# Optimization experiments

Measured on AMD Instinct MI355X. Metric: run time of the kernel, lower is better.

Reference implementation:

```python
import jax, jax.numpy as jnp
import numpy as np
from jax import lax

B, T, H, W, C = 2, 16, 64, 64, 64
KT, K = 3, 3


def kernel_to_freq_3d(kernel, T, H, W):
    # kernel: (C, k_t, k_h, k_w) -> (C, T, H, W) complex freq response
    Cc, k_t, k_h, k_w = kernel.shape
    t_idx = (jnp.arange(k_t) - k_t // 2) % T
    h_idx = (jnp.arange(k_h) - k_h // 2) % H
    w_idx = (jnp.arange(k_w) - k_w // 2) % W
    tt, th, tw = jnp.meshgrid(t_idx, h_idx, w_idx, indexing='ij')
    padded = jnp.zeros((Cc, T, H, W), dtype=kernel.dtype).at[:, tt, th, tw].set(kernel)
    return jnp.fft.fftn(padded, axes=(1, 2, 3))


def mamba_op(left, right):
    a1, b1 = left
    a2, b2 = right
    return (a1 * a2, a2 * b1 + b2)


def setup_inputs() -> dict:
    key = jax.random.key(0)
    ks = jax.random.split(key, 8)
    fan_in = KT * K * K
    x = jax.random.normal(ks[0], (B, T, H, W, C), dtype=jnp.float32)
    A_kernel = jax.random.normal(ks[1], (C, KT, K, K), dtype=jnp.float32) / np.sqrt(fan_in)
    B_kernel = jax.random.normal(ks[2], (C, KT, K, K), dtype=jnp.float32) / np.sqrt(fan_in)
    forget_bias = jnp.full((C,), 2.0, dtype=jnp.float32)
    forget_scale = jnp.full((C,), 0.01, dtype=jnp.float32)
    input_bias = jnp.zeros((C,), dtype=jnp.float32)
    input_scale = jnp.full((C,), 0.01, dtype=jnp.float32)
    delta_W = jax.random.normal(ks[3], (C, C), dtype=jnp.float32) / np.sqrt(C)
    delta_b = jnp.zeros((C,), dtype=jnp.float32)
    return {"x": x, "A_kernel": A_kernel, "B_kernel": B_kernel,
            "forget_bias": forget_bias, "forget_scale": forget_scale,
            "input_bias": input_bias, "input_scale": input_scale,
            "delta_W": delta_W, "delta_b": delta_b}


def reference(x, A_kernel, B_kernel, forget_bias, forget_scale,
              input_bias, input_scale, delta_W, delta_b):
    Bb, Tt, Hh, Ww, Cc = x.shape
    # freq-domain kernels: (C,T,H,W) -> (T,1,H,W,C) for broadcasting over batch
    A_f = kernel_to_freq_3d(A_kernel, Tt, Hh, Ww).transpose(1, 2, 3, 0)[:, None]
    B_f = kernel_to_freq_3d(B_kernel, Tt, Hh, Ww).transpose(1, 2, 3, 0)[:, None]
    # input-dependent gates (real, elementwise per channel)
    forget_gate = jax.nn.sigmoid(forget_bias + forget_scale * x)
    input_gate = jax.nn.sigmoid(input_bias + input_scale * x)
    delta = jax.nn.softplus(jnp.einsum('bthwc,cd->bthwd', x, delta_W) + delta_b)
    x_f = jnp.fft.fftn(x, axes=(1, 2, 3))  # complex (B,T,H,W,C)
    # move time axis to front for the scan: (T,B,H,W,C)
    a_seq = forget_gate.transpose(1, 0, 2, 3, 4) * A_f
    b_seq = (input_gate.transpose(1, 0, 2, 3, 4)
             * delta.transpose(1, 0, 2, 3, 4)
             * B_f * x_f.transpose(1, 0, 2, 3, 4))
    _, h_all_f = lax.associative_scan(mamba_op, (a_seq, b_seq), axis=0)
    h_f = h_all_f.transpose(1, 0, 2, 3, 4)
    h = jnp.fft.ifftn(h_f, axes=(1, 2, 3)).real
    return h.astype(x.dtype)
```

## Files before the change

### kernel.cpp

```cpp
#include <hip/hip_runtime.h>
#include <math.h>

#define Bb 2
#define Tt 16
#define Hh 64
#define Ww 64
#define Cc 64
#define ST_ (Hh*Ww*Cc)
#define SH_ (Ww*Cc)
#define SB_ (Tt*Hh*Ww*Cc)
#define XELEMS (Bb*Tt*Hh*Ww*Cc)

#define TWO_PI 6.2831853071795864769f

typedef __attribute__((ext_vector_type(8))) short bf16x8;
typedef __attribute__((ext_vector_type(4))) float f32x4;

#define OFF_PRE  8388608u
#define OFF_TWF  8390656u
#define OFF_THF  8394752u
#define OFF_THI  8402944u
#define OFF_TWI  8411136u

__device__ __forceinline__ float2 cmul(float2 a, float2 b) {
    return make_float2(fmaf(a.x, b.x, -a.y * b.y), fmaf(a.x, b.y, a.y * b.x));
}
__device__ __forceinline__ float2 cadd(float2 a, float2 b) { return make_float2(a.x + b.x, a.y + b.y); }
__device__ __forceinline__ float2 csub(float2 a, float2 b) { return make_float2(a.x - b.x, a.y - b.y); }

__device__ __forceinline__ unsigned bfpack(float2 f) {
    unsigned r = __float_as_uint(f.x);
    unsigned i = __float_as_uint(f.y);
    r = (r + 0x7fffu + ((r >> 16) & 1u)) >> 16;
    i = (i + 0x7fffu + ((i >> 16) & 1u)) >> 16;
    return r | (i << 16);
}
__device__ __forceinline__ float2 bfunpack(unsigned u) {
    return make_float2(__uint_as_float(u << 16), __uint_as_float(u & 0xffff0000u));
}

template <int S>
__device__ __forceinline__ void fft4(float2& a, float2& b, float2& c, float2& d) {
    float2 t0 = cadd(a, c), t1 = csub(a, c);
    float2 t2 = cadd(b, d), t3 = csub(b, d);
    a = cadd(t0, t2);
    c = csub(t0, t2);
    b = make_float2(t1.x - (float)S * t3.y, t1.y + (float)S * t3.x);
    d = make_float2(t1.x + (float)S * t3.y, t1.y - (float)S * t3.x);
}

template <int S>
__device__ __forceinline__ void fft16(float2 v[16]) {
    const float CS[10] = {1.f, 0.92387953f, 0.70710678f, 0.38268343f, 0.f,
                          -0.38268343f, -0.70710678f, -0.92387953f, -1.f, -0.92387953f};
    const float SN[10] = {0.f, 0.38268343f, 0.70710678f, 0.92387953f, 1.f,
                          0.92387953f, 0.70710678f, 0.38268343f, 0.f, -0.38268343f};
    float2 A[4][4];
#pragma unroll
    for (int j = 0; j < 4; ++j) {
        A[j][0] = v[j]; A[j][1] = v[4 + j]; A[j][2] = v[8 + j]; A[j][3] = v[12 + j];
        fft4<S>(A[j][0], A[j][1], A[j][2], A[j][3]);
#pragma unroll
        for (int k0 = 0; k0 < 4; ++k0) {
            int m = j * k0;
            float2 tw = make_float2(CS[m], (float)S * SN[m]);
            A[j][k0] = cmul(A[j][k0], tw);
        }
    }
#pragma unroll
    for (int k0 = 0; k0 < 4; ++k0) {
        fft4<S>(A[0][k0], A[1][k0], A[2][k0], A[3][k0]);
        v[k0] = A[0][k0]; v[k0 + 4] = A[1][k0]; v[k0 + 8] = A[2][k0]; v[k0 + 12] = A[3][k0];
    }
}

__global__ __launch_bounds__(256) void k_setup(const float* __restrict__ dW,
                                               unsigned* __restrict__ ws) {
    int j = blockIdx.x * 256 + threadIdx.x;
    if (j < 2048) {
        int p2 = j & 3, lane = (j >> 2) & 63, ka = (j >> 8) & 1, nt = j >> 9;
        int kb = ka * 32 + (lane >> 4) * 8 + 2 * p2;
        int ccol = (lane & 15) + 16 * nt;
        ws[OFF_PRE + j] = bfpack(make_float2(dW[kb * 64 + ccol], dW[(kb + 1) * 64 + ccol]));
        return;
    }
    int idx, table;
    if (j < 6144)       { idx = j - 2048;  table = 0; }
    else if (j < 14336) { idx = j - 6144;  table = 1; }
    else if (j < 22528) { idx = j - 14336; table = 2; }
    else                { idx = j - 22528; table = 3; }
    int p = idx & 3;
    int lane = (idx >> 2) & 63;
    int m = lane & 15, q = lane >> 4;
    int ka, r, reim;
    if (table == 0)      { ka = (idx >> 8) & 1; r = (idx >> 9) & 3;  reim = (idx >> 11) & 1; }
    else if (table == 3) { ka = (idx >> 8) & 3; r = (idx >> 10) & 3; reim = 0; }
    else                 { ka = (idx >> 8) & 3; r = (idx >> 10) & 3; reim = (idx >> 12) & 1; }
    int wp = r * 16 + m;
    int k0 = ka * 32 + q * 8 + 2 * p;
    float val[2];
#pragma unroll
    for (int dk = 0; dk < 2; ++dk) {
        int k = k0 + dk;
        float v;
        if (table == 0) {
            int a = (wp * k) & 63;
            float sn, cs; sincosf(TWO_PI * (float)a * (1.0f / 64.0f), &sn, &cs);
            v = (reim == 0) ? cs : -sn;
        } else {
            int h = k >> 1;
            int a = (wp * h) & 63;
            float sn, cs; sincosf(TWO_PI * (float)a * (1.0f / 64.0f), &sn, &cs);
            bool even = (k & 1) == 0;
            if (table == 1) {
                v = (reim == 0) ? (even ? cs : sn) : (even ? -sn : cs);
            } else if (table == 2) {
                v = (reim == 0) ? (even ? cs : -sn) : (even ? sn : cs);
                v *= (1.0f / 64.0f);
            } else {
                v = (even ? cs : -sn) * (1.0f / 64.0f);
            }
        }
        val[dk] = v;
    }
    unsigned base = (table == 0) ? OFF_TWF : (table == 1) ? OFF_THF
                  : (table == 2) ? OFF_THI : OFF_TWI;
    ws[base + idx] = bfpack(make_float2(val[0], val[1]));
}

__global__ __launch_bounds__(256) void k_dft_w_fwd(const float* __restrict__ x,
                                                   unsigned* __restrict__ X,
                                                   const uint4* __restrict__ T) {
    __shared__ float xsl[64 * 65];
    int tid = threadIdx.x;
    int sbase = blockIdx.x * 4096;
    for (int i = tid; i < 4096; i += 256)
        xsl[(i >> 6) * 65 + (i & 63)] = x[sbase + i];
    __syncthreads();

    int r = tid >> 6, lane = tid & 63;
    int m = lane & 15, q = lane >> 4;
    union U48 { uint4 u4; unsigned u[4]; bf16x8 v8; };
    U48 Are[2], Aim[2], Bf;
#pragma unroll
    for (int ka = 0; ka < 2; ++ka) {
        Are[ka].u4 = T[((0 * 4 + r) * 2 + ka) * 64 + lane];
        Aim[ka].u4 = T[((1 * 4 + r) * 2 + ka) * 64 + lane];
    }
    f32x4 ar[4], ai[4];
#pragma unroll
    for (int nt = 0; nt < 4; ++nt) { ar[nt] = (f32x4){0.f,0.f,0.f,0.f}; ai[nt] = (f32x4){0.f,0.f,0.f,0.f}; }
#pragma unroll
    for (int nt = 0; nt < 4; ++nt) {
        int cc = m + 16 * nt;
#pragma unroll
        for (int ka = 0; ka < 2; ++ka) {
            int w0 = ka * 32 + q * 8;
#pragma unroll
            for (int p = 0; p < 4; ++p)
                Bf.u[p] = bfpack(make_float2(xsl[(w0 + 2 * p) * 65 + cc],
                                             xsl[(w0 + 2 * p + 1) * 65 + cc]));
            ar[nt] = __builtin_amdgcn_mfma_f32_16x16x32_bf16(Are[ka].v8, Bf.v8, ar[nt], 0, 0, 0);
            ai[nt] = __builtin_amdgcn_mfma_f32_16x16x32_bf16(Aim[ka].v8, Bf.v8, ai[nt], 0, 0, 0);
        }
    }
#pragma unroll
    for (int nt = 0; nt < 4; ++nt) {
        int cc = m + 16 * nt;
#pragma unroll
        for (int reg = 0; reg < 4; ++reg) {
            int wp = r * 16 + q * 4 + reg;
            X[sbase + wp * 64 + cc] = bfpack(make_float2(ar[nt][reg], ai[nt][reg]));
        }
    }
}

__global__ __launch_bounds__(256) void k_dft_h(unsigned* __restrict__ X,
                                               const uint4* __restrict__ T) {
    __shared__ unsigned zs[64 * 68];
    int tid = threadIdx.x;
    int s = blockIdx.x;
    int bt = s >> 6, w = s & 63;
    int base = bt * ST_ + w * 64;
    for (int i = tid; i < 4096; i += 256)
        zs[(i >> 6) * 68 + (i & 63)] = X[base + (i >> 6) * SH_ + (i & 63)];
    __syncthreads();

    int r = tid >> 6, lane = tid & 63;
    int m = lane & 15, q = lane >> 4;
    union U48 { uint4 u4; unsigned u[4]; bf16x8 v8; };
    U48 Are[4], Aim[4], Bf;
#pragma unroll
    for (int ka = 0; ka < 4; ++ka) {
        Are[ka].u4 = T[((0 * 4 + r) * 4 + ka) * 64 + lane];
        Aim[ka].u4 = T[((1 * 4 + r) * 4 + ka) * 64 + lane];
    }
    f32x4 ar[4], ai[4];
#pragma unroll
    for (int nt = 0; nt < 4; ++nt) { ar[nt] = (f32x4){0.f,0.f,0.f,0.f}; ai[nt] = (f32x4){0.f,0.f,0.f,0.f}; }
#pragma unroll
    for (int nt = 0; nt < 4; ++nt) {
        int cc = m + 16 * nt;
#pragma unroll
        for (int ka = 0; ka < 4; ++ka) {
            int h0 = ka * 16 + q * 4;
            Bf.u[0] = zs[(h0 + 0) * 68 + cc];
            Bf.u[1] = zs[(h0 + 1) * 68 + cc];
            Bf.u[2] = zs[(h0 + 2) * 68 + cc];
            Bf.u[3] = zs[(h0 + 3) * 68 + cc];
            ar[nt] = __builtin_amdgcn_mfma_f32_16x16x32_bf16(Are[ka].v8, Bf.v8, ar[nt], 0, 0, 0);
            ai[nt] = __builtin_amdgcn_mfma_f32_16x16x32_bf16(Aim[ka].v8, Bf.v8, ai[nt], 0, 0, 0);
        }
    }
#pragma unroll
    for (int nt = 0; nt < 4; ++nt) {
        int cc = m + 16 * nt;
#pragma unroll
        for (int reg = 0; reg < 4; ++reg) {
            int hp = r * 16 + q * 4 + reg;
            X[base + hp * SH_ + cc] = bfpack(make_float2(ar[nt][reg], ai[nt][reg]));
        }
    }
}

__global__ __launch_bounds__(256) void k_dft_w_inv(const unsigned* __restrict__ X,
                                                   float* __restrict__ out,
                                                   const uint4* __restrict__ T) {
    __shared__ unsigned zs[64 * 68];
    int tid = threadIdx.x;
    int sbase = blockIdx.x * 4096;
    for (int i = tid; i < 4096; i += 256)
        zs[(i >> 6) * 68 + (i & 63)] = X[sbase + i];
    __syncthreads();

    int r = tid >> 6, lane = tid & 63;
    int m = lane & 15, q = lane >> 4;
    union U48 { uint4 u4; unsigned u[4]; bf16x8 v8; };
    U48 Are[4], Bf;
#pragma unroll
    for (int ka = 0; ka < 4; ++ka)
        Are[ka].u4 = T[(r * 4 + ka) * 64 + lane];
    f32x4 ar[4];
#pragma unroll
    for (int nt = 0; nt < 4; ++nt) ar[nt] = (f32x4){0.f,0.f,0.f,0.f};
#pragma unroll
    for (int nt = 0; nt < 4; ++nt) {
        int cc = m + 16 * nt;
#pragma unroll
        for (int ka = 0; ka < 4; ++ka) {
            int w0 = ka * 16 + q * 4;
            Bf.u[0] = zs[(w0 + 0) * 68 + cc];
            Bf.u[1] = zs[(w0 + 1) * 68 + cc];
            Bf.u[2] = zs[(w0 + 2) * 68 + cc];
            Bf.u[3] = zs[(w0 + 3) * 68 + cc];
            ar[nt] = __builtin_amdgcn_mfma_f32_16x16x32_bf16(Are[ka].v8, Bf.v8, ar[nt], 0, 0, 0);
        }
    }
#pragma unroll
    for (int nt = 0; nt < 4; ++nt) {
        int cc = m + 16 * nt;
#pragma unroll
        for (int reg = 0; reg < 4; ++reg) {
            int wp = r * 16 + q * 4 + reg;
            out[sbase + wp * 64 + cc] = ar[nt][reg];
        }
    }
}

__global__ __launch_bounds__(256) void k_mid(
    const float* __restrict__ x, unsigned* __restrict__ X,
    const float* __restrict__ Ak, const float* __restrict__ Bk,
    const float* __restrict__ fb, const float* __restrict__ fs,
    const float* __restrict__ ib, const float* __restrict__ isc_,
    const uint4* __restrict__ pre, const float* __restrict__ db) {
    const float CT[16] = {1.f, 0.9238795f, 0.7071068f, 0.3826834f, 0.f, -0.3826834f,
                          -0.7071068f, -0.9238795f, -1.f, -0.9238795f, -0.7071068f,
                          -0.3826834f, 0.f, 0.3826834f, 0.7071068f, 0.9238795f};
    const float SN[16] = {0.f, 0.3826834f, 0.7071068f, 0.9238795f, 1.f, 0.9238795f,
                          0.7071068f, 0.3826834f, 0.f, -0.3826834f, -0.7071068f,
                          -0.9238795f, -1.f, -0.9238795f, -0.7071068f, -0.3826834f};
    __shared__ float Akl[1728], Bkl[1728];
    __shared__ __align__(16) float xs[4][16 * 68 + 4];

    int tid = threadIdx.x;
    int g = tid >> 6, lane = tid & 63;
    int c = lane;
    int site = blockIdx.x * 4 + g;
    int b = site >> 12, hw = site & 4095;
    int h = hw >> 6, w = hw & 63;
    int base = b * SB_ + hw * 64;

    for (int i = tid; i < 1728; i += 256) { Akl[i] = Ak[i]; Bkl[i] = Bk[i]; }

    float xv[16];
    float2 v[16];
#pragma unroll
    for (int t = 0; t < 16; ++t) {
        xv[t] = x[base + t * ST_ + c];
        v[t] = bfunpack(X[base + t * ST_ + c]);
    }
#pragma unroll
    for (int t = 0; t < 16; ++t) xs[g][t * 68 + c] = xv[t];
    __syncthreads();

    int m = lane & 15, q = lane >> 4;
    bf16x8 Afrag[2];
#pragma unroll
    for (int ka = 0; ka < 2; ++ka) {
        int d0 = ka * 32 + q * 8;
        const float* p = &xs[g][m * 68 + d0];
        float4 f0 = *(const float4*)p;
        float4 f1 = *(const float4*)(p + 4);
        union { bf16x8 v8; unsigned u[4]; } U;
        U.u[0] = bfpack(make_float2(f0.x, f0.y));
        U.u[1] = bfpack(make_float2(f0.z, f0.w));
        U.u[2] = bfpack(make_float2(f1.x, f1.y));
        U.u[3] = bfpack(make_float2(f1.z, f1.w));
        Afrag[ka] = U.v8;
    }
#pragma unroll
    for (int nt = 0; nt < 4; ++nt) {
        int ccol = m + 16 * nt;
        float dbn = db[ccol];
        f32x4 acc = {dbn, dbn, dbn, dbn};
#pragma unroll
        for (int ka = 0; ka < 2; ++ka) {
            union { bf16x8 v8; uint4 u4; } Ub;
            Ub.u4 = pre[(nt * 2 + ka) * 64 + lane];
            acc = __builtin_amdgcn_mfma_f32_16x16x32_bf16(Afrag[ka], Ub.v8, acc, 0, 0, 0);
        }
#pragma unroll
        for (int reg = 0; reg < 4; ++reg)
            xs[g][(q * 4 + reg) * 68 + ccol] = acc[reg];
    }

    float sh, ch; sincosf(TWO_PI * (float)h / 64.0f, &sh, &ch);
    float sw, cw; sincosf(TWO_PI * (float)w / 64.0f, &sw, &cw);
    float2 eh[3] = { make_float2(ch, sh), make_float2(1.f, 0.f), make_float2(ch, -sh) };
    float2 ew[3] = { make_float2(cw, sw), make_float2(1.f, 0.f), make_float2(cw, -sw) };
    float2 GA[3], GB[3];
#pragma unroll
    for (int kt = 0; kt < 3; ++kt) { GA[kt] = make_float2(0.f, 0.f); GB[kt] = make_float2(0.f, 0.f); }
#pragma unroll
    for (int kh = 0; kh < 3; ++kh) {
#pragma unroll
        for (int kw = 0; kw < 3; ++kw) {
            float2 e = cmul(eh[kh], ew[kw]);
#pragma unroll
            for (int kt = 0; kt < 3; ++kt) {
                float ka = Akl[c * 27 + kt * 9 + kh * 3 + kw];
                float kb = Bkl[c * 27 + kt * 9 + kh * 3 + kw];
                GA[kt].x = fmaf(ka, e.x, GA[kt].x);
                GA[kt].y = fmaf(ka, e.y, GA[kt].y);
                GB[kt].x = fmaf(kb, e.x, GB[kt].x);
                GB[kt].y = fmaf(kb, e.y, GB[kt].y);
            }
        }
    }
    float fbc = fb[c], fsc = fs[c], ibc = ib[c], iscv = isc_[c];

    fft16<-1>(v);
    __syncthreads();

    float delta_raw[16];
#pragma unroll
    for (int t = 0; t < 16; ++t) delta_raw[t] = xs[g][t * 68 + c];

    float2 hv = make_float2(0.f, 0.f);
#pragma unroll
    for (int t = 0; t < 16; ++t) {
        float ct = CT[t], st = SN[t];
        float2 Af, Bf;
        Af.x = GA[1].x + ct * (GA[0].x + GA[2].x) - st * (GA[0].y - GA[2].y);
        Af.y = GA[1].y + ct * (GA[0].y + GA[2].y) + st * (GA[0].x - GA[2].x);
        Bf.x = GB[1].x + ct * (GB[0].x + GB[2].x) - st * (GB[0].y - GB[2].y);
        Bf.y = GB[1].y + ct * (GB[0].y + GB[2].y) + st * (GB[0].x - GB[2].x);

        float xc = xv[t];
        float fg  = __builtin_amdgcn_rcpf(1.f + __expf(-(fbc + fsc * xc)));
        float igv = __builtin_amdgcn_rcpf(1.f + __expf(-(ibc + iscv * xc)));
        float dot = delta_raw[t];
        float delta = (dot > 20.f) ? dot : __logf(1.f + __expf(dot));

        float sR = igv * delta;
        float2 bbv;
        bbv.x = sR * (Bf.x * v[t].x - Bf.y * v[t].y);
        bbv.y = sR * (Bf.x * v[t].y + Bf.y * v[t].x);
        float2 av = make_float2(fg * Af.x, fg * Af.y);
        float2 nh;
        nh.x = av.x * hv.x - av.y * hv.y + bbv.x;
        nh.y = av.x * hv.y + av.y * hv.x + bbv.y;
        hv = nh;
        v[t] = hv;
    }

    fft16<1>(v);

#pragma unroll
    for (int t = 0; t < 16; ++t) {
        float2 o = make_float2(v[t].x * 0.0625f, v[t].y * 0.0625f);
        X[base + t * ST_ + c] = bfpack(o);
    }
}

extern "C" void kernel_launch(void* const* d_in, const int* in_sizes, int n_in,
                              void* d_out, int out_size, void* d_ws, size_t ws_size,
                              hipStream_t stream) {
    const float* x   = (const float*)d_in[0];
    const float* Ak  = (const float*)d_in[1];
    const float* Bk  = (const float*)d_in[2];
    const float* fb  = (const float*)d_in[3];
    const float* fs  = (const float*)d_in[4];
    const float* ib  = (const float*)d_in[5];
    const float* is_ = (const float*)d_in[6];
    const float* dW  = (const float*)d_in[7];
    const float* db  = (const float*)d_in[8];
    float* out = (float*)d_out;
    unsigned* ws = (unsigned*)d_ws;
    unsigned* X = ws;

    k_setup<<<104, 256, 0, stream>>>(dW, ws);
    k_dft_w_fwd<<<Bb * Tt * Hh, 256, 0, stream>>>(x, X, (const uint4*)(ws + OFF_TWF));
    k_dft_h<<<Bb * Tt * Ww, 256, 0, stream>>>(X, (const uint4*)(ws + OFF_THF));
    k_mid<<<(Bb * Hh * Ww) / 4, 256, 0, stream>>>(x, X, Ak, Bk, fb, fs, ib, is_,
                                                  (const uint4*)(ws + OFF_PRE), db);
    k_dft_h<<<Bb * Tt * Ww, 256, 0, stream>>>(X, (const uint4*)(ws + OFF_THI));
    k_dft_w_inv<<<Bb * Tt * Hh, 256, 0, stream>>>(X, out, (const uint4*)(ws + OFF_TWI));
}
```

Measured before the change: 186.1 us.

## Ping-pong DFT stages through transposed intermediate layouts for contiguous reads

Each DFT stage now writes its output into a second workspace buffer in a transposed layout, so the next stage reads a contiguous 4096-element slab instead of doing a strided gather. k_mid reads its time series contiguously from the new layout and writes in the layout the inverse H pass expects. The forward W pass now converts x to bf16 while staging it in shared memory, and the MFMA B-fragments are loaded with vector uint2 LDS reads from a channel-major tile. The cost is twice the workspace and scattered strided global writes at the end of each stage.

```diff
diff --git a/kernel.cpp b/kernel.cpp
--- a/kernel.cpp
+++ b/kernel.cpp
@@ -7,20 +7,20 @@
 #define Ww 64
 #define Cc 64
 #define ST_ (Hh*Ww*Cc)
-#define SH_ (Ww*Cc)
 #define SB_ (Tt*Hh*Ww*Cc)
-#define XELEMS (Bb*Tt*Hh*Ww*Cc)
 
 #define TWO_PI 6.2831853071795864769f
 
 typedef __attribute__((ext_vector_type(8))) short bf16x8;
 typedef __attribute__((ext_vector_type(4))) float f32x4;
 
-#define OFF_PRE  8388608u
-#define OFF_TWF  8390656u
-#define OFF_THF  8394752u
-#define OFF_THI  8402944u
-#define OFF_TWI  8411136u
+#define BUF_A    0u
+#define BUF_B    8388608u
+#define OFF_PRE  16777216u
+#define OFF_TWF  16779264u
+#define OFF_THF  16783360u
+#define OFF_THI  16791552u
+#define OFF_TWI  16799744u
 
 __device__ __forceinline__ float2 cmul(float2 a, float2 b) {
     return make_float2(fmaf(a.x, b.x, -a.y * b.y), fmaf(a.x, b.y, a.y * b.x));
@@ -129,18 +129,21 @@
 }
 
 __global__ __launch_bounds__(256) void k_dft_w_fwd(const float* __restrict__ x,
-                                                   unsigned* __restrict__ X,
+                                                   unsigned* __restrict__ X1,
                                                    const uint4* __restrict__ T) {
-    __shared__ float xsl[64 * 65];
+    __shared__ unsigned zw[64 * 66];
     int tid = threadIdx.x;
-    int sbase = blockIdx.x * 4096;
-    for (int i = tid; i < 4096; i += 256)
-        xsl[(i >> 6) * 65 + (i & 63)] = x[sbase + i];
+    int s = blockIdx.x;
+    const float* src = x + (size_t)s * 4096;
+    for (int idx = tid; idx < 2048; idx += 256) {
+        int i = idx >> 6, c = idx & 63;
+        zw[c * 66 + i] = bfpack(make_float2(src[i * 128 + c], src[i * 128 + 64 + c]));
+    }
     __syncthreads();
 
     int r = tid >> 6, lane = tid & 63;
     int m = lane & 15, q = lane >> 4;
-    union U48 { uint4 u4; unsigned u[4]; bf16x8 v8; };
+    union U48 { uint4 u4; uint2 u2[2]; unsigned u[4]; bf16x8 v8; };
     U48 Are[2], Aim[2], Bf;
 #pragma unroll
     for (int ka = 0; ka < 2; ++ka) {
@@ -155,40 +158,42 @@
         int cc = m + 16 * nt;
 #pragma unroll
         for (int ka = 0; ka < 2; ++ka) {
-            int w0 = ka * 32 + q * 8;
-#pragma unroll
-            for (int p = 0; p < 4; ++p)
-                Bf.u[p] = bfpack(make_float2(xsl[(w0 + 2 * p) * 65 + cc],
-                                             xsl[(w0 + 2 * p + 1) * 65 + cc]));
+            int i0 = ka * 16 + q * 4;
+            Bf.u2[0] = *(const uint2*)&zw[cc * 66 + i0];
+            Bf.u2[1] = *(const uint2*)&zw[cc * 66 + i0 + 2];
             ar[nt] = __builtin_amdgcn_mfma_f32_16x16x32_bf16(Are[ka].v8, Bf.v8, ar[nt], 0, 0, 0);
             ai[nt] = __builtin_amdgcn_mfma_f32_16x16x32_bf16(Aim[ka].v8, Bf.v8, ai[nt], 0, 0, 0);
         }
     }
+    int bt = s >> 6, h = s & 63;
+    size_t ob = (size_t)bt * 262144 + (size_t)h * 64;
 #pragma unroll
     for (int nt = 0; nt < 4; ++nt) {
         int cc = m + 16 * nt;
 #pragma unroll
         for (int reg = 0; reg < 4; ++reg) {
             int wp = r * 16 + q * 4 + reg;
-            X[sbase + wp * 64 + cc] = bfpack(make_float2(ar[nt][reg], ai[nt][reg]));
-        }
-    }
-}
-
-__global__ __launch_bounds__(256) void k_dft_h(unsigned* __restrict__ X,
-                                               const uint4* __restrict__ T) {
-    __shared__ unsigned zs[64 * 68];
+            X1[ob + (size_t)wp * 4096 + cc] = bfpack(make_float2(ar[nt][reg], ai[nt][reg]));
+        }
+    }
+}
+
+__global__ __launch_bounds__(256) void k_dft_h_fwd(const unsigned* __restrict__ X1,
+                                                   unsigned* __restrict__ X2,
+                                                   const uint4* __restrict__ T) {
+    __shared__ unsigned zs[64 * 66];
     int tid = threadIdx.x;
     int s = blockIdx.x;
-    int bt = s >> 6, w = s & 63;
-    int base = bt * ST_ + w * 64;
-    for (int i = tid; i < 4096; i += 256)
-        zs[(i >> 6) * 68 + (i & 63)] = X[base + (i >> 6) * SH_ + (i & 63)];
+    const unsigned* src = X1 + (size_t)s * 4096;
+    for (int i = tid; i < 4096; i += 256) {
+        int h = i >> 6, c = i & 63;
+        zs[c * 66 + h] = src[i];
+    }
     __syncthreads();
 
     int r = tid >> 6, lane = tid & 63;
     int m = lane & 15, q = lane >> 4;
-    union U48 { uint4 u4; unsigned u[4]; bf16x8 v8; };
+    union U48 { uint4 u4; uint2 u2[2]; unsigned u[4]; bf16x8 v8; };
     U48 Are[4], Aim[4], Bf;
 #pragma unroll
     for (int ka = 0; ka < 4; ++ka) {
@@ -204,38 +209,91 @@
 #pragma unroll
         for (int ka = 0; ka < 4; ++ka) {
             int h0 = ka * 16 + q * 4;
-            Bf.u[0] = zs[(h0 + 0) * 68 + cc];
-            Bf.u[1] = zs[(h0 + 1) * 68 + cc];
-            Bf.u[2] = zs[(h0 + 2) * 68 + cc];
-            Bf.u[3] = zs[(h0 + 3) * 68 + cc];
+            Bf.u2[0] = *(const uint2*)&zs[cc * 66 + h0];
+            Bf.u2[1] = *(const uint2*)&zs[cc * 66 + h0 + 2];
             ar[nt] = __builtin_amdgcn_mfma_f32_16x16x32_bf16(Are[ka].v8, Bf.v8, ar[nt], 0, 0, 0);
             ai[nt] = __builtin_amdgcn_mfma_f32_16x16x32_bf16(Aim[ka].v8, Bf.v8, ai[nt], 0, 0, 0);
         }
     }
+    int b = s >> 10, t = (s >> 6) & 15, w = s & 63;
+    size_t ob = (size_t)b * 4194304 + (size_t)w * 1024 + (size_t)t * 64;
 #pragma unroll
     for (int nt = 0; nt < 4; ++nt) {
         int cc = m + 16 * nt;
 #pragma unroll
         for (int reg = 0; reg < 4; ++reg) {
             int hp = r * 16 + q * 4 + reg;
-            X[base + hp * SH_ + cc] = bfpack(make_float2(ar[nt][reg], ai[nt][reg]));
-        }
-    }
-}
-
-__global__ __launch_bounds__(256) void k_dft_w_inv(const unsigned* __restrict__ X,
+            X2[ob + (size_t)hp * 65536 + cc] = bfpack(make_float2(ar[nt][reg], ai[nt][reg]));
+        }
+    }
+}
+
+__global__ __launch_bounds__(256) void k_dft_h_inv(const unsigned* __restrict__ X3,
+                                                   unsigned* __restrict__ X4,
+                                                   const uint4* __restrict__ T) {
+    __shared__ unsigned zs[64 * 66];
+    int tid = threadIdx.x;
+    int s = blockIdx.x;
+    const unsigned* src = X3 + (size_t)s * 4096;
+    for (int i = tid; i < 4096; i += 256) {
+        int h = i >> 6, c = i & 63;
+        zs[c * 66 + h] = src[i];
+    }
+    __syncthreads();
+
+    int r = tid >> 6, lane = tid & 63;
+    int m = lane & 15, q = lane >> 4;
+    union U48 { uint4 u4; uint2 u2[2]; unsigned u[4]; bf16x8 v8; };
+    U48 Are[4], Aim[4], Bf;
+#pragma unroll
+    for (int ka = 0; ka < 4; ++ka) {
+        Are[ka].u4 = T[((0 * 4 + r) * 4 + ka) * 64 + lane];
+        Aim[ka].u4 = T[((1 * 4 + r) * 4 + ka) * 64 + lane];
+    }
+    f32x4 ar[4], ai[4];
+#pragma unroll
+    for (int nt = 0; nt < 4; ++nt) { ar[nt] = (f32x4){0.f,0.f,0.f,0.f}; ai[nt] = (f32x4){0.f,0.f,0.f,0.f}; }
+#pragma unroll
+    for (int nt = 0; nt < 4; ++nt) {
+        int cc = m + 16 * nt;
+#pragma unroll
+        for (int ka = 0; ka < 4; ++ka) {
+            int h0 = ka * 16 + q * 4;
+            Bf.u2[0] = *(const uint2*)&zs[cc * 66 + h0];
+            Bf.u2[1] = *(const uint2*)&zs[cc * 66 + h0 + 2];
+            ar[nt] = __builtin_amdgcn_mfma_f32_16x16x32_bf16(Are[ka].v8, Bf.v8, ar[nt], 0, 0, 0);
+            ai[nt] = __builtin_amdgcn_mfma_f32_16x16x32_bf16(Aim[ka].v8, Bf.v8, ai[nt], 0, 0, 0);
+        }
+    }
+    int bt = s >> 6, w = s & 63;
+    size_t ob = (size_t)bt * 262144 + (size_t)w * 64;
+#pragma unroll
+    for (int nt = 0; nt < 4; ++nt) {
+        int cc = m + 16 * nt;
+#pragma unroll
+        for (int reg = 0; reg < 4; ++reg) {
+            int hp = r * 16 + q * 4 + reg;
+            X4[ob + (size_t)hp * 4096 + cc] = bfpack(make_float2(ar[nt][reg], ai[nt][reg]));
+        }
+    }
+}
+
+__global__ __launch_bounds__(256) void k_dft_w_inv(const unsigned* __restrict__ X4,
                                                    float* __restrict__ out,
                                                    const uint4* __restrict__ T) {
-    __shared__ unsigned zs[64 * 68];
+    __shared__ unsigned zs[64 * 66];
     int tid = threadIdx.x;
-    int sbase = blockIdx.x * 4096;
-    for (int i = tid; i < 4096; i += 256)
-        zs[(i >> 6) * 68 + (i & 63)] = X[sbase + i];
+    int s = blockIdx.x;
+    const unsigned* src = X4 + (size_t)s * 4096;
+    for (int i = tid; i < 4096; i += 256) {
+        int w = i >> 6, c = i & 63;
+        zs[c * 66 + w] = src[i];
+    }
     __syncthreads();
 
     int r = tid >> 6, lane = tid & 63;
     int m = lane & 15, q = lane >> 4;
-    union U48 { uint4 u4; unsigned u[4]; bf16x8 v8; };
+    union U48 { uint4 u4; uint2 u2[2]; unsigned u[4]; bf16x8 v8; };
     U48 Are[4], Bf;
 #pragma unroll
     for (int ka = 0; ka < 4; ++ka)
@@ -249,26 +307,26 @@
 #pragma unroll
         for (int ka = 0; ka < 4; ++ka) {
             int w0 = ka * 16 + q * 4;
-            Bf.u[0] = zs[(w0 + 0) * 68 + cc];
-            Bf.u[1] = zs[(w0 + 1) * 68 + cc];
-            Bf.u[2] = zs[(w0 + 2) * 68 + cc];
-            Bf.u[3] = zs[(w0 + 3) * 68 + cc];
+            Bf.u2[0] = *(const uint2*)&zs[cc * 66 + w0];
+            Bf.u2[1] = *(const uint2*)&zs[cc * 66 + w0 + 2];
             ar[nt] = __builtin_amdgcn_mfma_f32_16x16x32_bf16(Are[ka].v8, Bf.v8, ar[nt], 0, 0, 0);
         }
     }
+    float* dst = out + (size_t)s * 4096;
 #pragma unroll
     for (int nt = 0; nt < 4; ++nt) {
         int cc = m + 16 * nt;
 #pragma unroll
         for (int reg = 0; reg < 4; ++reg) {
             int wp = r * 16 + q * 4 + reg;
-            out[sbase + wp * 64 + cc] = ar[nt][reg];
+            dst[wp * 64 + cc] = ar[nt][reg];
         }
     }
 }
 
 __global__ __launch_bounds__(256) void k_mid(
-    const float* __restrict__ x, unsigned* __restrict__ X,
+    const float* __restrict__ x, const unsigned* __restrict__ X2,
+    unsigned* __restrict__ X3,
     const float* __restrict__ Ak, const float* __restrict__ Bk,
     const float* __restrict__ fb, const float* __restrict__ fs,
     const float* __restrict__ ib, const float* __restrict__ isc_,
@@ -288,16 +346,17 @@
     int site = blockIdx.x * 4 + g;
     int b = site >> 12, hw = site & 4095;
     int h = hw >> 6, w = hw & 63;
-    int base = b * SB_ + hw * 64;
+    size_t base = (size_t)b * SB_ + (size_t)hw * 64;
 
     for (int i = tid; i < 1728; i += 256) { Akl[i] = Ak[i]; Bkl[i] = Bk[i]; }
 
     float xv[16];
     float2 v[16];
+    const unsigned* src2 = X2 + (size_t)site * 1024;
 #pragma unroll
     for (int t = 0; t < 16; ++t) {
-        xv[t] = x[base + t * ST_ + c];
-        v[t] = bfunpack(X[base + t * ST_ + c]);
+        xv[t] = x[base + (size_t)t * ST_ + c];
+        v[t] = bfunpack(src2[t * 64 + c]);
     }
 #pragma unroll
     for (int t = 0; t < 16; ++t) xs[g][t * 68 + c] = xv[t];
@@ -396,10 +455,11 @@
 
     fft16<1>(v);
 
+    size_t ob = (size_t)b * 4194304 + (size_t)w * 4096 + (size_t)h * 64 + c;
 #pragma unroll
     for (int t = 0; t < 16; ++t) {
         float2 o = make_float2(v[t].x * 0.0625f, v[t].y * 0.0625f);
-        X[base + t * ST_ + c] = bfpack(o);
+        X3[ob + (size_t)t * 262144] = bfpack(o);
     }
 }
 
@@ -417,13 +477,14 @@
     const float* db  = (const float*)d_in[8];
     float* out = (float*)d_out;
     unsigned* ws = (unsigned*)d_ws;
-    unsigned* X = ws;
+    unsigned* A = ws + BUF_A;
+    unsigned* B = ws + BUF_B;
 
     k_setup<<<104, 256, 0, stream>>>(dW, ws);
-    k_dft_w_fwd<<<Bb * Tt * Hh, 256, 0, stream>>>(x, X, (const uint4*)(ws + OFF_TWF));
-    k_dft_h<<<Bb * Tt * Ww, 256, 0, stream>>>(X, (const uint4*)(ws + OFF_THF));
-    k_mid<<<(Bb * Hh * Ww) / 4, 256, 0, stream>>>(x, X, Ak, Bk, fb, fs, ib, is_,
+    k_dft_w_fwd<<<Bb * Tt * Hh, 256, 0, stream>>>(x, A, (const uint4*)(ws + OFF_TWF));
+    k_dft_h_fwd<<<Bb * Tt * Ww, 256, 0, stream>>>(A, B, (const uint4*)(ws + OFF_THF));
+    k_mid<<<(Bb * Hh * Ww) / 4, 256, 0, stream>>>(x, B, A, Ak, Bk, fb, fs, ib, is_,
                                                   (const uint4*)(ws + OFF_PRE), db);
-    k_dft_h<<<Bb * Tt * Ww, 256, 0, stream>>>(X, (const uint4*)(ws + OFF_THI));
-    k_dft_w_inv<<<Bb * Tt * Hh, 256, 0, stream>>>(X, out, (const uint4*)(ws + OFF_TWI));
-}
+    k_dft_h_inv<<<Bb * Tt * Ww, 256, 0, stream>>>(A, B, (const uint4*)(ws + OFF_THI));
+    k_dft_w_inv<<<Bb * Tt * Hh, 256, 0, stream>>>(B, out, (const uint4*)(ws + OFF_TWI));
+}
```

Result: faster. 171.7 us (-7.7%).
